# Optimization experiments

Hardware: AMD Instinct MI355X
Metric: run time of the kernel (lower is better)

The kernel has to match this reference:

```python
import jax, jax.numpy as jnp
import numpy as np

B, S, D_IN, D_OUT = 4, 2048, 2048, 8192


def setup_inputs() -> dict:
    key = jax.random.key(0)
    k1, k2 = jax.random.split(key)
    x = jax.random.normal(k1, (B, S, D_IN), dtype=jnp.float32)
    weight = jax.random.normal(k2, (D_OUT, D_IN), dtype=jnp.float32) * 0.02
    alpha = jnp.float32(1.0)
    bias = jnp.zeros((D_OUT,), dtype=jnp.float32)
    return {"x": x, "weight": weight, "alpha": alpha, "bias": bias}


def reference(x, weight, alpha, bias):
    # Ternary quantization: delta = 0.7 * mean(|w|); w_q in {-1,0,1} * alpha
    delta = 0.7 * jnp.mean(jnp.abs(weight))
    w_t = jnp.where(weight > delta, jnp.float32(1.0),
                    jnp.where(weight < -delta, jnp.float32(-1.0), jnp.float32(0.0)))
    w_q = w_t * alpha  # [out, in]
    # F.linear: x @ w_q^T + bias
    return jnp.einsum('bsd,od->bso', x, w_q) + bias
```

## Files before the change

### kernel.cpp

```cpp
#include <hip/hip_runtime.h>
#include <hip/hip_bf16.h>
#include <stdint.h>

typedef __attribute__((ext_vector_type(4))) int i32x4;
typedef signed char s8;

#define M_TOT 8192
#define N_TOT 8192
#define K_TOT 2048
#define W_COUNT (N_TOT * K_TOT)
#define X_COUNT (M_TOT * K_TOT)

__global__ void tl_reduce(const float* __restrict__ w, const float* __restrict__ x,
                          double* __restrict__ wsum, float* __restrict__ xmax) {
    const int b = blockIdx.x;
    if (b < 1024) {
        const int tid = b * 256 + threadIdx.x;
        const float4* w4 = (const float4*)w;
        double s = 0.0;
        for (int i = tid; i < W_COUNT / 4; i += 1024 * 256) {
            float4 v = w4[i];
            s += (double)fabsf(v.x) + (double)fabsf(v.y) + (double)fabsf(v.z) + (double)fabsf(v.w);
        }
        #pragma unroll
        for (int off = 32; off > 0; off >>= 1) s += __shfl_down(s, off);
        __shared__ double red[4];
        if ((threadIdx.x & 63) == 0) red[threadIdx.x >> 6] = s;
        __syncthreads();
        if (threadIdx.x == 0) wsum[b] = (red[0] + red[1]) + (red[2] + red[3]);
    } else {
        const int tid = (b - 1024) * 256 + threadIdx.x;
        const float4* x4 = (const float4*)x;
        float m = 0.0f;
        for (int i = tid; i < X_COUNT / 4; i += 1024 * 256) {
            float4 v = x4[i];
            m = fmaxf(m, fmaxf(fmaxf(fabsf(v.x), fabsf(v.y)), fmaxf(fabsf(v.z), fabsf(v.w))));
        }
        #pragma unroll
        for (int off = 32; off > 0; off >>= 1) m = fmaxf(m, __shfl_down(m, off));
        __shared__ float redm[4];
        if ((threadIdx.x & 63) == 0) redm[threadIdx.x >> 6] = m;
        __syncthreads();
        if (threadIdx.x == 0) xmax[b - 1024] = fmaxf(fmaxf(redm[0], redm[1]), fmaxf(redm[2], redm[3]));
    }
}

__global__ void tl_finalize(const double* __restrict__ wsum, const float* __restrict__ xmax,
                            const float* __restrict__ alpha,
                            double* __restrict__ delta, float* __restrict__ qp) {
    const int t = threadIdx.x;
    double s = (wsum[t] + wsum[t + 256]) + (wsum[t + 512] + wsum[t + 768]);
    float m = fmaxf(fmaxf(xmax[t], xmax[t + 256]), fmaxf(xmax[t + 512], xmax[t + 768]));
    #pragma unroll
    for (int off = 32; off > 0; off >>= 1) {
        s += __shfl_down(s, off);
        m = fmaxf(m, __shfl_down(m, off));
    }
    __shared__ double rs[4];
    __shared__ float rm[4];
    if ((t & 63) == 0) { rs[t >> 6] = s; rm[t >> 6] = m; }
    __syncthreads();
    if (t == 0) {
        *delta = 0.7 * (((rs[0] + rs[1]) + (rs[2] + rs[3])) / (double)W_COUNT);
        float mm = fmaxf(fmaxf(rm[0], rm[1]), fmaxf(rm[2], rm[3]));
        qp[0] = 127.0f / mm;
        qp[1] = alpha[0] * (mm / 127.0f);
    }
}

__global__ void tl_tern_w(const float* __restrict__ w, const double* __restrict__ delta_p,
                          s8* __restrict__ wb) {
    const double d = *delta_p;
    const int i = (blockIdx.x * 256 + threadIdx.x) * 16;
    union { s8 c[16]; i32x4 v; } o;
    #pragma unroll
    for (int j = 0; j < 16; j += 4) {
        float4 v = *(const float4*)(w + i + j);
        float f[4] = {v.x, v.y, v.z, v.w};
        #pragma unroll
        for (int r = 0; r < 4; ++r) {
            double wd = (double)f[r];
            o.c[j + r] = wd > d ? 1 : (wd < -d ? -1 : 0);
        }
    }
    *(i32x4*)(wb + i) = o.v;
}

__global__ void tl_quant_x(const float* __restrict__ x, const float* __restrict__ qp,
                           s8* __restrict__ xb) {
    const float inv = qp[0];
    const int i = (blockIdx.x * 256 + threadIdx.x) * 16;
    union { s8 c[16]; i32x4 v; } o;
    #pragma unroll
    for (int j = 0; j < 16; j += 4) {
        float4 v = *(const float4*)(x + i + j);
        float f[4] = {v.x, v.y, v.z, v.w};
        #pragma unroll
        for (int r = 0; r < 4; ++r) {
            int q = (int)__builtin_rintf(f[r] * inv);
            q = q > 127 ? 127 : (q < -127 ? -127 : q);
            o.c[j + r] = (s8)q;
        }
    }
    *(i32x4*)(xb + i) = o.v;
}


#define SB    __builtin_amdgcn_sched_barrier(0)
#define BARR  __builtin_amdgcn_s_barrier()
#define LGKM0 asm volatile("s_waitcnt lgkmcnt(0)" ::: "memory")
#define VMW(N) asm volatile("s_waitcnt vmcnt(" #N ")" ::: "memory")

#define GLDS(SRC, DOFF) __builtin_amdgcn_global_load_lds(                      \
    (const __attribute__((address_space(1))) void*)(SRC),                      \
    (__attribute__((address_space(3))) void*)(lds + (DOFF)), 16, 0, 0)

#define RD_A(S, G) do {                                                        \
    _Pragma("unroll") for (int m_ = 0; m_ < 4; ++m_)                           \
        aF[m_] = *(const i32x4*)(lds + (S) * 16384 + wrOff + ((G) * 4 + m_) * 1024 + lrd); \
} while (0)

#define RD_B(S) do {                                                           \
    _Pragma("unroll") for (int n_ = 0; n_ < 4; ++n_)                           \
        bF[n_] = *(const i32x4*)(lds + 49152 + (S) * 16384 + wcOff + n_ * 1024 + lrd); \
} while (0)

#define MM(G) do {                                                             \
    _Pragma("unroll") for (int m_ = 0; m_ < 4; ++m_)                           \
    _Pragma("unroll") for (int n_ = 0; n_ < 4; ++n_)                           \
        acc[(G) * 4 + m_][n_] = __builtin_amdgcn_mfma_i32_16x16x64_i8(         \
            aF[m_], bF[n_], acc[(G) * 4 + m_][n_], 0, 0, 0);                   \
} while (0)

#define KTILE(S, SSTG, KOFF, DOSTG, GATE) do {                                 \
    RD_A(S, 0); RD_B(S);                                                       \
    if (DOSTG) { GLDS(aSrc + (KOFF), (SSTG) * 16384 + L);                      \
                 GLDS(bSrc + (KOFF), 49152 + (SSTG) * 16384 + L); }            \
    SB; BARR; LGKM0; SB;                                                       \
    __builtin_amdgcn_s_setprio(1); MM(0); __builtin_amdgcn_s_setprio(0); SB; BARR; \
    RD_A(S, 1);                                                                \
    if (DOSTG) { GLDS(aSrc + (KOFF) + 262144, (SSTG) * 16384 + 8192 + L);      \
                 GLDS(bSrc + (KOFF) + 262144, 49152 + (SSTG) * 16384 + 8192 + L); } \
    SB; BARR; LGKM0; SB;                                                       \
    __builtin_amdgcn_s_setprio(1); MM(1); __builtin_amdgcn_s_setprio(0); SB;   \
    GATE; BARR;                                                                \
} while (0)

__global__ __launch_bounds__(512, 2) void tl_gemm_i8(
    const s8* __restrict__ A, const s8* __restrict__ Bm,
    const float* __restrict__ qp, const float* __restrict__ bias,
    float* __restrict__ C) {
    __shared__ __attribute__((aligned(128))) char lds[98304];

    const int t = threadIdx.x;
    const int wid = t >> 6;
    const int l = t & 63;
    const int wr = wid >> 2;
    const int wc = wid & 3;

    const int bid = blockIdx.x;
    const int x = bid & 7;
    const int j = bid >> 3;
    const int tm = x * 4 + ((j >> 3) & 3);
    const int tn = (j >> 5) * 8 + (j & 7);
    const int row0 = tm * 256, col0 = tn * 256;

    const int L = t * 16;
    const int off = L ^ (((L >> 6) & 3) << 4);
    const int sr = off >> 6;
    const int kb = off & 63;
    const s8* aSrc = A + (size_t)(row0 + sr) * K_TOT + kb;
    const s8* bSrc = Bm + (size_t)(col0 + sr) * K_TOT + kb;

    const int rlane = l & 15, kq = l >> 4;
    const int lrd = rlane * 64 + ((kq ^ (rlane & 3)) << 4);
    const int wrOff = wr * 8192;
    const int wcOff = wc * 4096;

    i32x4 acc[8][4] = {};
    i32x4 aF[4], bF[4];

    GLDS(aSrc, L);                    GLDS(bSrc, 49152 + L);
    GLDS(aSrc + 262144, 8192 + L);    GLDS(bSrc + 262144, 49152 + 8192 + L);
    GLDS(aSrc + 64, 16384 + L);       GLDS(bSrc + 64, 49152 + 16384 + L);
    GLDS(aSrc + 64 + 262144, 16384 + 8192 + L);
    GLDS(bSrc + 64 + 262144, 49152 + 16384 + 8192 + L);
    VMW(4); BARR;

    int koff = 128;
    #pragma unroll 1
    for (int i = 0; i < 10; ++i) {
        KTILE(0, 2, koff, 1, VMW(4)); koff += 64;
        KTILE(1, 0, koff, 1, VMW(4)); koff += 64;
        KTILE(2, 1, koff, 1, VMW(4)); koff += 64;
    }
    KTILE(0, 0, 0, 0, VMW(0));
    KTILE(1, 0, 0, 0, (void)0);

    const float osc = qp[1];
    const int crow = row0 + wr * 128 + kq * 4;
    const int ccol = col0 + wc * 64 + rlane;
    #pragma unroll
    for (int fn = 0; fn < 4; ++fn) {
        const float bv = bias[ccol + fn * 16];
        #pragma unroll
        for (int fm = 0; fm < 8; ++fm) {
            #pragma unroll
            for (int r = 0; r < 4; ++r) {
                C[(size_t)(crow + fm * 16 + r) * N_TOT + (ccol + fn * 16)] =
                    (float)acc[fm][fn][r] * osc + bv;
            }
        }
    }
}

extern "C" void kernel_launch(void* const* d_in, const int* in_sizes, int n_in,
                              void* d_out, int out_size, void* d_ws, size_t ws_size,
                              hipStream_t stream) {
    const float* x     = (const float*)d_in[0];
    const float* wgt   = (const float*)d_in[1];
    const float* alpha = (const float*)d_in[2];
    const float* bias  = (const float*)d_in[3];
    float* out = (float*)d_out;

    char* ws = (char*)d_ws;
    double* wsum = (double*)ws;
    float* xmax  = (float*)(ws + 8192);
    double* delta = (double*)(ws + 12288);
    float* qp     = (float*)(ws + 12304);
    s8* xb = (s8*)(ws + 16384);
    s8* wb = (s8*)(ws + 16384 + (size_t)X_COUNT);

    tl_reduce<<<2048, 256, 0, stream>>>(wgt, x, wsum, xmax);
    tl_finalize<<<1, 256, 0, stream>>>(wsum, xmax, alpha, delta, qp);
    tl_tern_w<<<W_COUNT / (256 * 16), 256, 0, stream>>>(wgt, delta, wb);
    tl_quant_x<<<X_COUNT / (256 * 16), 256, 0, stream>>>(x, qp, xb);
    tl_gemm_i8<<<(M_TOT / 256) * (N_TOT / 256), 512, 0, stream>>>(xb, wb, qp, bias, out);
}
```

Measured before the change: 230.5 us.

## Switch int8 GEMM to 32x32x32 MFMA tiles with new LDS swizzle

Replaces the 16x16x64 int8 MFMA with the 32x32x32 variant, so each wave computes 4x2 32x32 blocks instead of 8x4 16x16 blocks. The LDS read pattern and swizzle are reworked to match, K is split into two 32-wide halves per tile, and the global-to-LDS staging order changes so A is loaded in the first half and B in the second. Larger MFMA tiles cut the number of LDS fragment reads per MAC. Launch bounds drop to one block per CU, which lowers the occupancy hint but gives more register headroom for the 16-wide accumulators.

```diff
diff --git a/kernel.cpp b/kernel.cpp
--- a/kernel.cpp
+++ b/kernel.cpp
@@ -3,6 +3,7 @@
 #include <stdint.h>
 
 typedef __attribute__((ext_vector_type(4))) int i32x4;
+typedef __attribute__((ext_vector_type(16))) int i32x16;
 typedef signed char s8;
 
 #define M_TOT 8192
@@ -115,38 +116,42 @@
     (const __attribute__((address_space(1))) void*)(SRC),                      \
     (__attribute__((address_space(3))) void*)(lds + (DOFF)), 16, 0, 0)
 
-#define RD_A(S, G) do {                                                        \
+#define RD_A(S, KK) do {                                                       \
     _Pragma("unroll") for (int m_ = 0; m_ < 4; ++m_)                           \
-        aF[m_] = *(const i32x4*)(lds + (S) * 16384 + wrOff + ((G) * 4 + m_) * 1024 + lrd); \
-} while (0)
-
-#define RD_B(S) do {                                                           \
-    _Pragma("unroll") for (int n_ = 0; n_ < 4; ++n_)                           \
-        bF[n_] = *(const i32x4*)(lds + 49152 + (S) * 16384 + wcOff + n_ * 1024 + lrd); \
-} while (0)
-
-#define MM(G) do {                                                             \
+        aF[m_] = *(const i32x4*)(lds + (S) * 16384 + wrOff + m_ * 2048 +       \
+                                 (lrd ^ ((KK) * 32)));                         \
+} while (0)
+
+#define RD_B(S, KK) do {                                                       \
+    _Pragma("unroll") for (int n_ = 0; n_ < 2; ++n_)                           \
+        bF[n_] = *(const i32x4*)(lds + 49152 + (S) * 16384 + wcOff + n_ * 2048 + \
+                                 (lrd ^ ((KK) * 32)));                         \
+} while (0)
+
+#define MM() do {                                                              \
     _Pragma("unroll") for (int m_ = 0; m_ < 4; ++m_)                           \
-    _Pragma("unroll") for (int n_ = 0; n_ < 4; ++n_)                           \
-        acc[(G) * 4 + m_][n_] = __builtin_amdgcn_mfma_i32_16x16x64_i8(         \
-            aF[m_], bF[n_], acc[(G) * 4 + m_][n_], 0, 0, 0);                   \
+    _Pragma("unroll") for (int n_ = 0; n_ < 2; ++n_)                           \
+        acc[m_][n_] = __builtin_amdgcn_mfma_i32_32x32x32_i8(                   \
+            aF[m_], bF[n_], acc[m_][n_], 0, 0, 0);                             \
 } while (0)
 
 #define KTILE(S, SSTG, KOFF, DOSTG, GATE) do {                                 \
-    RD_A(S, 0); RD_B(S);                                                       \
+                            \
+    RD_A(S, 0); RD_B(S, 0);                                                    \
     if (DOSTG) { GLDS(aSrc + (KOFF), (SSTG) * 16384 + L);                      \
-                 GLDS(bSrc + (KOFF), 49152 + (SSTG) * 16384 + L); }            \
+                 GLDS(aSrc + (KOFF) + 262144, (SSTG) * 16384 + 8192 + L); }    \
     SB; BARR; LGKM0; SB;                                                       \
-    __builtin_amdgcn_s_setprio(1); MM(0); __builtin_amdgcn_s_setprio(0); SB; BARR; \
-    RD_A(S, 1);                                                                \
-    if (DOSTG) { GLDS(aSrc + (KOFF) + 262144, (SSTG) * 16384 + 8192 + L);      \
+    __builtin_amdgcn_s_setprio(1); MM(); __builtin_amdgcn_s_setprio(0); SB; BARR; \
+                                        \
+    RD_A(S, 1); RD_B(S, 1);                                                    \
+    if (DOSTG) { GLDS(bSrc + (KOFF), 49152 + (SSTG) * 16384 + L);              \
                  GLDS(bSrc + (KOFF) + 262144, 49152 + (SSTG) * 16384 + 8192 + L); } \
     SB; BARR; LGKM0; SB;                                                       \
-    __builtin_amdgcn_s_setprio(1); MM(1); __builtin_amdgcn_s_setprio(0); SB;   \
+    __builtin_amdgcn_s_setprio(1); MM(); __builtin_amdgcn_s_setprio(0); SB;    \
     GATE; BARR;                                                                \
 } while (0)
 
-__global__ __launch_bounds__(512, 2) void tl_gemm_i8(
+__global__ __launch_bounds__(512, 1) void tl_gemm_i8(
     const s8* __restrict__ A, const s8* __restrict__ Bm,
     const float* __restrict__ qp, const float* __restrict__ bias,
     float* __restrict__ C) {
@@ -166,24 +171,24 @@
     const int row0 = tm * 256, col0 = tn * 256;
 
     const int L = t * 16;
-    const int off = L ^ (((L >> 6) & 3) << 4);
+    const int off = L ^ (((L >> 7) & 3) << 4);
     const int sr = off >> 6;
     const int kb = off & 63;
     const s8* aSrc = A + (size_t)(row0 + sr) * K_TOT + kb;
     const s8* bSrc = Bm + (size_t)(col0 + sr) * K_TOT + kb;
 
-    const int rlane = l & 15, kq = l >> 4;
-    const int lrd = rlane * 64 + ((kq ^ (rlane & 3)) << 4);
+    const int rl = l & 31, kg = l >> 5;
+    const int lrd = rl * 64 + ((kg ^ ((rl >> 1) & 3)) << 4);
     const int wrOff = wr * 8192;
     const int wcOff = wc * 4096;
 
-    i32x4 acc[8][4] = {};
-    i32x4 aF[4], bF[4];
-
-    GLDS(aSrc, L);                    GLDS(bSrc, 49152 + L);
-    GLDS(aSrc + 262144, 8192 + L);    GLDS(bSrc + 262144, 49152 + 8192 + L);
-    GLDS(aSrc + 64, 16384 + L);       GLDS(bSrc + 64, 49152 + 16384 + L);
-    GLDS(aSrc + 64 + 262144, 16384 + 8192 + L);
+    i32x16 acc[4][2] = {};
+    i32x4 aF[4], bF[2];
+
+    GLDS(aSrc, L);                    GLDS(aSrc + 262144, 8192 + L);
+    GLDS(bSrc, 49152 + L);            GLDS(bSrc + 262144, 49152 + 8192 + L);
+    GLDS(aSrc + 64, 16384 + L);       GLDS(aSrc + 64 + 262144, 16384 + 8192 + L);
+    GLDS(bSrc + 64, 49152 + 16384 + L);
     GLDS(bSrc + 64 + 262144, 49152 + 16384 + 8192 + L);
     VMW(4); BARR;
 
@@ -198,17 +203,17 @@
     KTILE(1, 0, 0, 0, (void)0);
 
     const float osc = qp[1];
-    const int crow = row0 + wr * 128 + kq * 4;
-    const int ccol = col0 + wc * 64 + rlane;
-    #pragma unroll
-    for (int fn = 0; fn < 4; ++fn) {
-        const float bv = bias[ccol + fn * 16];
-        #pragma unroll
-        for (int fm = 0; fm < 8; ++fm) {
+    #pragma unroll
+    for (int m_ = 0; m_ < 4; ++m_) {
+        const int crow = row0 + wr * 128 + m_ * 32 + kg * 4;
+        #pragma unroll
+        for (int n_ = 0; n_ < 2; ++n_) {
+            const int ccol = col0 + wc * 64 + n_ * 32 + rl;
+            const float bv = bias[ccol];
             #pragma unroll
-            for (int r = 0; r < 4; ++r) {
-                C[(size_t)(crow + fm * 16 + r) * N_TOT + (ccol + fn * 16)] =
-                    (float)acc[fm][fn][r] * osc + bv;
+            for (int r = 0; r < 16; ++r) {
+                const int row = crow + (r & 3) + 8 * (r >> 2);
+                C[(size_t)row * N_TOT + ccol] = (float)acc[m_][n_][r] * osc + bv;
             }
         }
     }
```

Result: faster. 212.3 us (-7.9%).
